# Kernel tuning notes

Hardware: AMD Instinct MI355X
Metric: run time of the kernel (lower is better)

The kernel has to match this reference:

```python
import jax, jax.numpy as jnp
import numpy as np

ALPHA, BETA, BASE, MARGIN = 2.0, 50.0, 0.5, 0.1
B, D, N_CLASSES = 8192, 128, 512


def setup_inputs() -> dict:
    key = jax.random.key(0)
    k1, k2 = jax.random.split(key)
    emb = jax.random.normal(k1, (B, D), dtype=jnp.float32)
    emb = emb / jnp.linalg.norm(emb, axis=1, keepdims=True)  # L2-normalized as documented
    labels = jax.random.randint(k2, (B,), 0, N_CLASSES, dtype=jnp.int32)
    return {"embeddings": emb, "labels": labels}


def reference(embeddings, labels):
    sim = embeddings @ embeddings.T  # (B, B)
    b = embeddings.shape[0]
    same = labels[:, None] == labels[None, :]
    eye = jnp.eye(b, dtype=bool)
    pos_mask = same & ~eye
    neg_mask = ~same

    # per-row extrema over masked entries (inf sentinels make empty rows inert)
    pos_min = jnp.min(jnp.where(pos_mask, sim, jnp.inf), axis=1)   # (B,)
    neg_max = jnp.max(jnp.where(neg_mask, sim, -jnp.inf), axis=1)  # (B,)

    # hard-pair mining
    hard_pos = pos_mask & (sim - MARGIN < neg_max[:, None])
    hard_neg = neg_mask & (sim + MARGIN > pos_min[:, None])

    valid = (pos_mask.any(axis=1) & neg_mask.any(axis=1)
             & hard_pos.any(axis=1) & hard_neg.any(axis=1))

    pos_sum = jnp.sum(jnp.where(hard_pos, jnp.exp(-ALPHA * (sim - BASE)), 0.0), axis=1)
    neg_sum = jnp.sum(jnp.where(hard_neg, jnp.exp(BETA * (sim - BASE)), 0.0), axis=1)
    row_loss = jnp.log1p(pos_sum) / ALPHA + jnp.log1p(neg_sum) / BETA

    n_valid = jnp.sum(valid)
    loss = jnp.sum(jnp.where(valid, row_loss, 0.0)) / jnp.maximum(n_valid, 1).astype(row_loss.dtype)
    return loss
```

## Files before the change

kernel.cpp:

```cpp
#include <hip/hip_runtime.h>
#include <hip/hip_bf16.h>

#define NB 8192
#define ND 128

static constexpr float F_ALPHA  = 2.0f;
static constexpr float F_BETA   = 50.0f;
static constexpr float F_BASE   = 0.5f;
static constexpr float F_MARGIN = 0.1f;
static constexpr float LOG2E    = 1.4426950408889634f;
static constexpr float C1P = -F_ALPHA * LOG2E, C0P =  F_ALPHA * F_BASE * LOG2E;
static constexpr float C1N =  F_BETA  * LOG2E, C0N = -F_BETA  * F_BASE * LOG2E;

typedef __attribute__((ext_vector_type(8))) short short8;
typedef __attribute__((ext_vector_type(4))) float f32x4;

__device__ __forceinline__ unsigned fenc(float f) {
  unsigned u = __float_as_uint(f);
  return (u & 0x80000000u) ? ~u : (u | 0x80000000u);
}
__device__ __forceinline__ float fdec(unsigned k) {
  unsigned u = (k & 0x80000000u) ? (k & 0x7FFFFFFFu) : ~k;
  return __uint_as_float(u);
}

__device__ __forceinline__ void async16(const void* g, void* l) {
  __builtin_amdgcn_global_load_lds(
      (const __attribute__((address_space(1))) void*)g,
      (__attribute__((address_space(3))) void*)l, 16, 0, 0);
}

__global__ void k_convert(const float4* __restrict__ in, char* __restrict__ P,
                          const int* __restrict__ lab,
                          unsigned* __restrict__ pmKey, unsigned* __restrict__ nmKey,
                          float* __restrict__ pSum, float* __restrict__ nSum,
                          int* __restrict__ cnt) {
  int i = blockIdx.x * 256 + threadIdx.x;
  float4 v = in[i];
  __hip_bfloat16 a = __float2bfloat16(v.x), b = __float2bfloat16(v.y),
                 c = __float2bfloat16(v.z), d = __float2bfloat16(v.w);
  ushort4 o;
  o.x = *(unsigned short*)&a; o.y = *(unsigned short*)&b;
  o.z = *(unsigned short*)&c; o.w = *(unsigned short*)&d;
  const int row = i >> 5, c4 = i & 31;
  const int g = row >> 4, r15 = row & 15;
  const int kk = c4 >> 3, q = (c4 >> 1) & 3, j = (c4 & 1) * 4;
  *(ushort4*)(P + (((g * 4 + kk) * 64 + q * 16 + r15) * 16 + j * 2)) = o;
  if (i < NB) {
    pmKey[i] = 0xFFFFFFFFu;
    nmKey[i] = 0u;
    pSum[i]  = 0.f;
    nSum[i]  = 0.f;
    atomicAdd(&cnt[lab[i]], 1);
  }
}

template<int PASS>
__global__ __launch_bounds__(256, 2)
void k_simpass(const char* __restrict__ P,
               const int* __restrict__ lab,
               unsigned* __restrict__ pmKey,
               unsigned* __restrict__ nmKey,
               float* __restrict__ pSum,
               float* __restrict__ nSum,
               float* __restrict__ selfSim)
{
  __shared__ __align__(16) char sB[2][8192];

  const int t    = threadIdx.x;
  const int lane = t & 63, wid = t >> 6;
  const int q    = lane >> 4, r15 = lane & 15;
  const int rBase = blockIdx.y * 128 + wid * 32;
  const int cBase = blockIdx.x * 512;

  const char* gB = P + (size_t)cBase * 256;

  async16(gB + wid * 1024 + lane * 16,        &sB[0][0] + wid * 1024);
  async16(gB + 4096 + wid * 1024 + lane * 16, &sB[0][0] + 4096 + wid * 1024);

  short8 afr[4][2];
#pragma unroll
  for (int mi = 0; mi < 2; ++mi) {
    const char* pa = P + (size_t)(((rBase >> 4) + mi) * 4) * 1024 + lane * 16;
#pragma unroll
    for (int kk = 0; kk < 4; ++kk)
      afr[kk][mi] = *(const short8*)(pa + kk * 1024);
  }

  int lrr[8]; float pmr[8], nmr[8];
#pragma unroll
  for (int mi = 0; mi < 2; ++mi)
#pragma unroll
    for (int rg = 0; rg < 4; ++rg) {
      int r = rBase + mi * 16 + q * 4 + rg;
      lrr[mi * 4 + rg] = lab[r];
      if (PASS == 1) {
        pmr[mi * 4 + rg] = fdec(pmKey[r]) - F_MARGIN;
        nmr[mi * 4 + rg] = fdec(nmKey[r]) + F_MARGIN;
      }
    }

  float st1[8], st2[8];
#pragma unroll
  for (int i = 0; i < 8; ++i) {
    st1[i] = (PASS == 0) ?  __builtin_inff() : 0.f;
    st2[i] = (PASS == 0) ? -__builtin_inff() : 0.f;
  }

  int clN0 = lab[cBase + r15];
  int clN1 = lab[cBase + 16 + r15];

  const f32x4 Z4 = (f32x4){0.f, 0.f, 0.f, 0.f};

  __syncthreads();

#pragma unroll 1
  for (int ct = 0; ct < 16; ++ct) {
    const int buf = ct & 1;
    const int cTile = cBase + ct * 32;

    if (ct < 15) {
      const char* gn = gB + (size_t)(ct + 1) * 8192;
      async16(gn + wid * 1024 + lane * 16,        &sB[buf ^ 1][0] + wid * 1024);
      async16(gn + 4096 + wid * 1024 + lane * 16, &sB[buf ^ 1][0] + 4096 + wid * 1024);
    }

    const char* sb = &sB[buf][0] + lane * 16;
    short8 b[8];
#pragma unroll
    for (int kk = 0; kk < 4; ++kk) {
      b[kk]     = *(const short8*)(sb + kk * 1024);
      b[4 + kk] = *(const short8*)(sb + 4096 + kk * 1024);
    }

    f32x4 acc[2][2];
#pragma unroll
    for (int mi = 0; mi < 2; ++mi) {
      acc[mi][0] = __builtin_amdgcn_mfma_f32_16x16x32_bf16(afr[0][mi], b[0], Z4, 0, 0, 0);
      acc[mi][1] = __builtin_amdgcn_mfma_f32_16x16x32_bf16(afr[0][mi], b[4], Z4, 0, 0, 0);
    }
#pragma unroll
    for (int kk = 1; kk < 4; ++kk)
#pragma unroll
      for (int mi = 0; mi < 2; ++mi) {
        acc[mi][0] = __builtin_amdgcn_mfma_f32_16x16x32_bf16(afr[kk][mi], b[kk],     acc[mi][0], 0, 0, 0);
        acc[mi][1] = __builtin_amdgcn_mfma_f32_16x16x32_bf16(afr[kk][mi], b[4 + kk], acc[mi][1], 0, 0, 0);
      }

    const int cl0 = clN0, cl1 = clN1;
    if (ct < 15) {
      clN0 = lab[cTile + 32 + r15];
      clN1 = lab[cTile + 48 + r15];
    }

#pragma unroll
    for (int mi = 0; mi < 2; ++mi)
#pragma unroll
      for (int rg = 0; rg < 4; ++rg) {
        const int idx = mi * 4 + rg;
        const int lr  = lrr[idx];
        const float s0 = acc[mi][0][rg], s1 = acc[mi][1][rg];
        const bool same0 = (lr == cl0), same1 = (lr == cl1);
        if (PASS == 0) {
          float x0 = same0 ? s0 :  __builtin_inff();
          float x1 = same1 ? s1 :  __builtin_inff();
          st1[idx] = fminf(fminf(st1[idx], x0), x1);
          float y0 = same0 ? -__builtin_inff() : s0;
          float y1 = same1 ? -__builtin_inff() : s1;
          st2[idx] = fmaxf(fmaxf(st2[idx], y0), y1);
        } else {
          float e0 = __builtin_amdgcn_exp2f(
              fmaf(s0, same0 ? C1P : C1N, same0 ? C0P : C0N));
          float e1 = __builtin_amdgcn_exp2f(
              fmaf(s1, same1 ? C1P : C1N, same1 ? C0P : C0N));
          bool hp0 = same0 && (s0 < nmr[idx]), hn0 = !same0 && (s0 > pmr[idx]);
          bool hp1 = same1 && (s1 < nmr[idx]), hn1 = !same1 && (s1 > pmr[idx]);
          st1[idx] += (hp0 ? e0 : 0.f) + (hp1 ? e1 : 0.f);
          st2[idx] += (hn0 ? e0 : 0.f) + (hn1 ? e1 : 0.f);
        }
      }

    if (PASS == 0 && cTile == rBase) {
#pragma unroll
      for (int mi = 0; mi < 2; ++mi)
#pragma unroll
        for (int rg = 0; rg < 4; ++rg)
          if (r15 == q * 4 + rg)
            selfSim[rBase + mi * 16 + q * 4 + rg] = acc[mi][mi][rg];
    }

    __syncthreads();
  }

#pragma unroll
  for (int mi = 0; mi < 2; ++mi)
#pragma unroll
    for (int rg = 0; rg < 4; ++rg) {
      const int idx = mi * 4 + rg;
      const int r   = rBase + mi * 16 + q * 4 + rg;
      float v1 = st1[idx], v2 = st2[idx];
      if (PASS == 0) {
#pragma unroll
        for (int d = 1; d < 16; d <<= 1) {
          v1 = fminf(v1, __shfl_xor(v1, d));
          v2 = fmaxf(v2, __shfl_xor(v2, d));
        }
        if (r15 == 0) {
          atomicMin(&pmKey[r], fenc(v1));
          atomicMax(&nmKey[r], fenc(v2));
        }
      } else {
#pragma unroll
        for (int d = 1; d < 16; d <<= 1) {
          v1 += __shfl_xor(v1, d);
          v2 += __shfl_xor(v2, d);
        }
        if (r15 == 0) {
          if (v1 != 0.f) atomicAdd(&pSum[r], v1);
          if (v2 != 0.f) atomicAdd(&nSum[r], v2);
        }
      }
    }
}

__global__ void k_final(const unsigned* __restrict__ pmKey,
                        const unsigned* __restrict__ nmKey,
                        const float* __restrict__ pSum,
                        const float* __restrict__ nSum,
                        const float* __restrict__ selfSim,
                        const int* __restrict__ lab,
                        const int* __restrict__ cnt,
                        float* __restrict__ out)
{
  const int t = threadIdx.x;
  float ls = 0.f, nv = 0.f;
  for (int r = t; r < NB; r += 1024) {
    int c = cnt[lab[r]];
    unsigned nk = nmKey[r];
    bool pe = (c > 1);
    bool ne = (c < NB) && (nk > 0x007FFFFFu);
    if (pe && ne) {
      float pm = fdec(pmKey[r]), nm = fdec(nk);
      if (pm - F_MARGIN < nm) {
        float ss = selfSim[r];
        float psub = (ss - F_MARGIN < nm)
                       ? __builtin_amdgcn_exp2f(fmaf(ss, C1P, C0P)) : 0.f;
        float ps = fmaxf(pSum[r] - psub, 0.f);
        ls += log1pf(ps) * (1.0f / F_ALPHA) + log1pf(nSum[r]) * (1.0f / F_BETA);
        nv += 1.f;
      }
    }
  }
#pragma unroll
  for (int d = 1; d < 64; d <<= 1) {
    ls += __shfl_xor(ls, d);
    nv += __shfl_xor(nv, d);
  }
  __shared__ float sL[16], sC[16];
  if ((t & 63) == 0) { sL[t >> 6] = ls; sC[t >> 6] = nv; }
  __syncthreads();
  if (t == 0) {
    float a = 0.f, c = 0.f;
#pragma unroll
    for (int w = 0; w < 16; ++w) { a += sL[w]; c += sC[w]; }
    out[0] = a / fmaxf(c, 1.f);
  }
}

extern "C" void kernel_launch(void* const* d_in, const int* in_sizes, int n_in,
                              void* d_out, int out_size, void* d_ws, size_t ws_size,
                              hipStream_t stream)
{
  const float* emb = (const float*)d_in[0];
  const int*   lab = (const int*)d_in[1];
  float* out = (float*)d_out;

  char* ws = (char*)d_ws;
  char*     P       = ws;
  unsigned* pmKey   = (unsigned*)(ws + 2097152);
  unsigned* nmKey   = (unsigned*)(ws + 2097152 + 32768);
  float*    pSum    = (float*)(ws + 2097152 + 65536);
  float*    nSum    = (float*)(ws + 2097152 + 98304);
  float*    selfSim = (float*)(ws + 2097152 + 131072);
  int*      cnt     = (int*)(ws + 2097152 + 163840);

  hipMemsetAsync(cnt, 0, 512 * sizeof(int), stream);
  k_convert<<<NB * ND / (256 * 4), 256, 0, stream>>>(
      (const float4*)emb, P, lab, pmKey, nmKey, pSum, nSum, cnt);

  dim3 grid(16, 64);
  k_simpass<0><<<grid, 256, 0, stream>>>(P, lab, pmKey, nmKey, pSum, nSum, selfSim);
  k_simpass<1><<<grid, 256, 0, stream>>>(P, lab, pmKey, nmKey, pSum, nSum, selfSim);
  k_final<<<1, 1024, 0, stream>>>(pmKey, nmKey, pSum, nSum, selfSim, lab, cnt, out);
}
```

Measured before the change: 93.05 us.

## Exploit similarity symmetry: compute upper-triangle tiles and scatter column reductions

Switches to 128x128 block tiles over a 64x64 grid and skips blocks below the diagonal. Each off-diagonal tile applies its results to both its rows and, through shared-memory column reductions and atomics, its columns, which roughly halves the MFMA and exp work in both passes. The per-row atomic arrays are padded with a stride of 4 to reduce atomic contention and false sharing. In exchange there are more atomics per column, extra per-tile shuffle and shared-memory work, and about half the launched blocks exit immediately.

Measured after the change: 162.4 us. +74.5%, slower.

```diff
diff --git a/kernel.cpp b/kernel.cpp
--- a/kernel.cpp
+++ b/kernel.cpp
@@ -3,6 +3,7 @@
 
 #define NB 8192
 #define ND 128
+#define STR 4
 
 static constexpr float F_ALPHA  = 2.0f;
 static constexpr float F_BETA   = 50.0f;
@@ -47,10 +48,10 @@
   const int kk = c4 >> 3, q = (c4 >> 1) & 3, j = (c4 & 1) * 4;
   *(ushort4*)(P + (((g * 4 + kk) * 64 + q * 16 + r15) * 16 + j * 2)) = o;
   if (i < NB) {
-    pmKey[i] = 0xFFFFFFFFu;
-    nmKey[i] = 0u;
-    pSum[i]  = 0.f;
-    nSum[i]  = 0.f;
+    pmKey[i * STR] = 0xFFFFFFFFu;
+    nmKey[i * STR] = 0u;
+    pSum[i * STR]  = 0.f;
+    nSum[i * STR]  = 0.f;
     atomicAdd(&cnt[lab[i]], 1);
   }
 }
@@ -65,18 +66,22 @@
                float* __restrict__ nSum,
                float* __restrict__ selfSim)
 {
-  __shared__ __align__(16) char sB[2][8192];
+  __shared__ __align__(16) char sB[32768];
+  __shared__ float sC1[4][128], sC2[4][128];
 
   const int t    = threadIdx.x;
   const int lane = t & 63, wid = t >> 6;
   const int q    = lane >> 4, r15 = lane & 15;
-  const int rBase = blockIdx.y * 128 + wid * 32;
-  const int cBase = blockIdx.x * 512;
+  const int br = blockIdx.y, bc = blockIdx.x;
+  if (bc < br) return;
+  const bool odg = (bc > br);
+  const int rBase = br * 128 + wid * 32;
+  const int cBase = bc * 128;
 
   const char* gB = P + (size_t)cBase * 256;
-
-  async16(gB + wid * 1024 + lane * 16,        &sB[0][0] + wid * 1024);
-  async16(gB + 4096 + wid * 1024 + lane * 16, &sB[0][0] + 4096 + wid * 1024);
+#pragma unroll
+  for (int ch = 0; ch < 8; ++ch)
+    async16(gB + ch * 4096 + t * 16, sB + ch * 4096 + wid * 1024);
 
   short8 afr[4][2];
 #pragma unroll
@@ -95,8 +100,8 @@
       int r = rBase + mi * 16 + q * 4 + rg;
       lrr[mi * 4 + rg] = lab[r];
       if (PASS == 1) {
-        pmr[mi * 4 + rg] = fdec(pmKey[r]) - F_MARGIN;
-        nmr[mi * 4 + rg] = fdec(nmKey[r]) + F_MARGIN;
+        pmr[mi * 4 + rg] = fdec(pmKey[r * STR]) - F_MARGIN;
+        nmr[mi * 4 + rg] = fdec(nmKey[r * STR]) + F_MARGIN;
       }
     }
 
@@ -107,25 +112,23 @@
     st2[i] = (PASS == 0) ? -__builtin_inff() : 0.f;
   }
 
-  int clN0 = lab[cBase + r15];
-  int clN1 = lab[cBase + 16 + r15];
-
   const f32x4 Z4 = (f32x4){0.f, 0.f, 0.f, 0.f};
-
   __syncthreads();
 
-#pragma unroll 1
-  for (int ct = 0; ct < 16; ++ct) {
-    const int buf = ct & 1;
+#pragma unroll
+  for (int ct = 0; ct < 4; ++ct) {
     const int cTile = cBase + ct * 32;
-
-    if (ct < 15) {
-      const char* gn = gB + (size_t)(ct + 1) * 8192;
-      async16(gn + wid * 1024 + lane * 16,        &sB[buf ^ 1][0] + wid * 1024);
-      async16(gn + 4096 + wid * 1024 + lane * 16, &sB[buf ^ 1][0] + 4096 + wid * 1024);
-    }
-
-    const char* sb = &sB[buf][0] + lane * 16;
+    const int c0 = cTile + r15, c1 = cTile + 16 + r15;
+    const int cl0 = lab[c0], cl1 = lab[c1];
+    float nmc0 = 0.f, nmc1 = 0.f, pmc0 = 0.f, pmc1 = 0.f;
+    if (PASS == 1 && odg) {
+      nmc0 = fdec(nmKey[c0 * STR]) + F_MARGIN;
+      nmc1 = fdec(nmKey[c1 * STR]) + F_MARGIN;
+      pmc0 = fdec(pmKey[c0 * STR]) - F_MARGIN;
+      pmc1 = fdec(pmKey[c1 * STR]) - F_MARGIN;
+    }
+
+    const char* sb = sB + ct * 8192 + lane * 16;
     short8 b[8];
 #pragma unroll
     for (int kk = 0; kk < 4; ++kk) {
@@ -147,11 +150,9 @@
         acc[mi][1] = __builtin_amdgcn_mfma_f32_16x16x32_bf16(afr[kk][mi], b[4 + kk], acc[mi][1], 0, 0, 0);
       }
 
-    const int cl0 = clN0, cl1 = clN1;
-    if (ct < 15) {
-      clN0 = lab[cTile + 32 + r15];
-      clN1 = lab[cTile + 48 + r15];
-    }
+    float stc1[2], stc2[2];
+    stc1[0] = stc1[1] = (PASS == 0) ?  __builtin_inff() : 0.f;
+    stc2[0] = stc2[1] = (PASS == 0) ? -__builtin_inff() : 0.f;
 
 #pragma unroll
     for (int mi = 0; mi < 2; ++mi)
@@ -168,6 +169,12 @@
           float y0 = same0 ? -__builtin_inff() : s0;
           float y1 = same1 ? -__builtin_inff() : s1;
           st2[idx] = fmaxf(fmaxf(st2[idx], y0), y1);
+          if (odg) {
+            stc1[0] = fminf(stc1[0], x0);
+            stc1[1] = fminf(stc1[1], x1);
+            stc2[0] = fmaxf(stc2[0], y0);
+            stc2[1] = fmaxf(stc2[1], y1);
+          }
         } else {
           float e0 = __builtin_amdgcn_exp2f(
               fmaf(s0, same0 ? C1P : C1N, same0 ? C0P : C0N));
@@ -177,10 +184,39 @@
           bool hp1 = same1 && (s1 < nmr[idx]), hn1 = !same1 && (s1 > pmr[idx]);
           st1[idx] += (hp0 ? e0 : 0.f) + (hp1 ? e1 : 0.f);
           st2[idx] += (hn0 ? e0 : 0.f) + (hn1 ? e1 : 0.f);
-        }
-      }
-
-    if (PASS == 0 && cTile == rBase) {
+          if (odg) {
+            bool hpc0 = same0 && (s0 < nmc0), hnc0 = !same0 && (s0 > pmc0);
+            bool hpc1 = same1 && (s1 < nmc1), hnc1 = !same1 && (s1 > pmc1);
+            stc1[0] += hpc0 ? e0 : 0.f;
+            stc1[1] += hpc1 ? e1 : 0.f;
+            stc2[0] += hnc0 ? e0 : 0.f;
+            stc2[1] += hnc1 ? e1 : 0.f;
+          }
+        }
+      }
+
+    if (odg) {
+#pragma unroll
+      for (int ni = 0; ni < 2; ++ni) {
+        float v1 = stc1[ni], v2 = stc2[ni];
+#pragma unroll
+        for (int d = 16; d < 64; d <<= 1) {
+          if (PASS == 0) {
+            v1 = fminf(v1, __shfl_xor(v1, d));
+            v2 = fmaxf(v2, __shfl_xor(v2, d));
+          } else {
+            v1 += __shfl_xor(v1, d);
+            v2 += __shfl_xor(v2, d);
+          }
+        }
+        if (q == 0) {
+          sC1[wid][ct * 32 + ni * 16 + r15] = v1;
+          sC2[wid][ct * 32 + ni * 16 + r15] = v2;
+        }
+      }
+    }
+
+    if (PASS == 0 && br == bc && ct == wid) {
 #pragma unroll
       for (int mi = 0; mi < 2; ++mi)
 #pragma unroll
@@ -188,8 +224,6 @@
           if (r15 == q * 4 + rg)
             selfSim[rBase + mi * 16 + q * 4 + rg] = acc[mi][mi][rg];
     }
-
-    __syncthreads();
   }
 
 #pragma unroll
@@ -206,8 +240,8 @@
           v2 = fmaxf(v2, __shfl_xor(v2, d));
         }
         if (r15 == 0) {
-          atomicMin(&pmKey[r], fenc(v1));
-          atomicMax(&nmKey[r], fenc(v2));
+          if (v1 <  __builtin_inff()) atomicMin(&pmKey[r * STR], fenc(v1));
+          if (v2 > -__builtin_inff()) atomicMax(&nmKey[r * STR], fenc(v2));
         }
       } else {
 #pragma unroll
@@ -216,11 +250,29 @@
           v2 += __shfl_xor(v2, d);
         }
         if (r15 == 0) {
-          if (v1 != 0.f) atomicAdd(&pSum[r], v1);
-          if (v2 != 0.f) atomicAdd(&nSum[r], v2);
-        }
-      }
-    }
+          if (v1 != 0.f) atomicAdd(&pSum[r * STR], v1);
+          if (v2 != 0.f) atomicAdd(&nSum[r * STR], v2);
+        }
+      }
+    }
+
+  if (odg) {
+    __syncthreads();
+    if (t < 128) {
+      const int col = cBase + t;
+      if (PASS == 0) {
+        float mn = fminf(fminf(sC1[0][t], sC1[1][t]), fminf(sC1[2][t], sC1[3][t]));
+        float mx = fmaxf(fmaxf(sC2[0][t], sC2[1][t]), fmaxf(sC2[2][t], sC2[3][t]));
+        if (mn <  __builtin_inff()) atomicMin(&pmKey[col * STR], fenc(mn));
+        if (mx > -__builtin_inff()) atomicMax(&nmKey[col * STR], fenc(mx));
+      } else {
+        float s1 = (sC1[0][t] + sC1[1][t]) + (sC1[2][t] + sC1[3][t]);
+        float s2 = (sC2[0][t] + sC2[1][t]) + (sC2[2][t] + sC2[3][t]);
+        if (s1 != 0.f) atomicAdd(&pSum[col * STR], s1);
+        if (s2 != 0.f) atomicAdd(&nSum[col * STR], s2);
+      }
+    }
+  }
 }
 
 __global__ void k_final(const unsigned* __restrict__ pmKey,
@@ -236,17 +288,17 @@
   float ls = 0.f, nv = 0.f;
   for (int r = t; r < NB; r += 1024) {
     int c = cnt[lab[r]];
-    unsigned nk = nmKey[r];
+    unsigned nk = nmKey[r * STR];
     bool pe = (c > 1);
     bool ne = (c < NB) && (nk > 0x007FFFFFu);
     if (pe && ne) {
-      float pm = fdec(pmKey[r]), nm = fdec(nk);
+      float pm = fdec(pmKey[r * STR]), nm = fdec(nk);
       if (pm - F_MARGIN < nm) {
         float ss = selfSim[r];
         float psub = (ss - F_MARGIN < nm)
                        ? __builtin_amdgcn_exp2f(fmaf(ss, C1P, C0P)) : 0.f;
-        float ps = fmaxf(pSum[r] - psub, 0.f);
-        ls += log1pf(ps) * (1.0f / F_ALPHA) + log1pf(nSum[r]) * (1.0f / F_BETA);
+        float ps = fmaxf(pSum[r * STR] - psub, 0.f);
+        ls += log1pf(ps) * (1.0f / F_ALPHA) + log1pf(nSum[r * STR]) * (1.0f / F_BETA);
         nv += 1.f;
       }
     }
@@ -278,17 +330,17 @@
   char* ws = (char*)d_ws;
   char*     P       = ws;
   unsigned* pmKey   = (unsigned*)(ws + 2097152);
-  unsigned* nmKey   = (unsigned*)(ws + 2097152 + 32768);
-  float*    pSum    = (float*)(ws + 2097152 + 65536);
-  float*    nSum    = (float*)(ws + 2097152 + 98304);
-  float*    selfSim = (float*)(ws + 2097152 + 131072);
-  int*      cnt     = (int*)(ws + 2097152 + 163840);
+  unsigned* nmKey   = (unsigned*)(ws + 2097152 + 131072);
+  float*    pSum    = (float*)(ws + 2097152 + 262144);
+  float*    nSum    = (float*)(ws + 2097152 + 393216);
+  float*    selfSim = (float*)(ws + 2097152 + 524288);
+  int*      cnt     = (int*)(ws + 2097152 + 557056);
 
   hipMemsetAsync(cnt, 0, 512 * sizeof(int), stream);
   k_convert<<<NB * ND / (256 * 4), 256, 0, stream>>>(
       (const float4*)emb, P, lab, pmKey, nmKey, pSum, nSum, cnt);
 
-  dim3 grid(16, 64);
+  dim3 grid(64, 64);
   k_simpass<0><<<grid, 256, 0, stream>>>(P, lab, pmKey, nmKey, pSum, nSum, selfSim);
   k_simpass<1><<<grid, 256, 0, stream>>>(P, lab, pmKey, nmKey, pSum, nSum, selfSim);
   k_final<<<1, 1024, 0, stream>>>(pmKey, nmKey, pSum, nSum, selfSim, lab, cnt, out);
```
